# Optimization experiments

Hardware: AMD Instinct MI355X
Metric: run time of the kernel (lower is better)

The kernel has to match this reference:

```python
import jax, jax.numpy as jnp
import numpy as np


def setup_inputs() -> dict:
    key = jax.random.key(0)
    k1, k2 = jax.random.split(key)
    B, C, D = 16384, 4096, 1024
    feat = jax.random.normal(k1, (B, D), dtype=jnp.float32)
    centers = jax.random.normal(k2, (C, D), dtype=jnp.float32)
    return {"feat": feat, "centers": centers}


def reference(feat, centers):
    # Pairwise squared Euclidean distance: dist[b, c] = sum_d (feat[b,d] - centers[c,d])^2
    # materializing the O(B*C*D) broadcast difference (same math as the torch module).
    x2 = jnp.sum(feat * feat, axis=-1, keepdims=True)          # [B, 1]
    c2 = jnp.sum(centers * centers, axis=-1)[None, :]          # [1, C]
    xc = jnp.einsum("bd,cd->bc", feat, centers)                # [B, C] GEMM
    dist = x2 + c2 - 2.0 * xc
    return dist
```

## Files before the change

kernel.cpp:

```cpp
#include <hip/hip_runtime.h>
#include <hip/hip_bf16.h>

typedef __bf16 bf16x8 __attribute__((ext_vector_type(8)));
typedef float floatx4 __attribute__((ext_vector_type(4)));

__device__ __forceinline__ unsigned short f2bf(float f) {
    unsigned u = __float_as_uint(f);
    u += 0x7FFFu + ((u >> 16) & 1u);
    return (unsigned short)(u >> 16);
}

__device__ __forceinline__ void gl2lds(const void* g, void* l) {
    void* gnc = const_cast<void*>(g);
    __builtin_amdgcn_global_load_lds(
        (__attribute__((address_space(1))) void*)gnc,
        (__attribute__((address_space(3))) void*)l,
        16, 0, 0);
}

__global__ __launch_bounds__(256) void cast_norm_kernel(
    const float* __restrict__ in, unsigned short* __restrict__ outb,
    float* __restrict__ norm)
{
    const int row = blockIdx.x;
    const int tid = threadIdx.x;
    const float4 v = ((const float4*)(in + (size_t)row * 1024))[tid];
    float s = v.x * v.x + v.y * v.y + v.z * v.z + v.w * v.w;
    ushort4 o;
    o.x = f2bf(v.x); o.y = f2bf(v.y); o.z = f2bf(v.z); o.w = f2bf(v.w);
    ((ushort4*)(outb + (size_t)row * 1024))[tid] = o;
#pragma unroll
    for (int off = 32; off > 0; off >>= 1) s += __shfl_down(s, off);
    __shared__ float ws[4];
    if ((tid & 63) == 0) ws[tid >> 6] = s;
    __syncthreads();
    if (tid == 0) norm[row] = ws[0] + ws[1] + ws[2] + ws[3];
}

__global__ __launch_bounds__(256) void dist_gemm(
    const unsigned short* __restrict__ A,
    const unsigned short* __restrict__ B,
    const float* __restrict__ x2,
    const float* __restrict__ c2,
    float* __restrict__ out,
    int M, int N)
{
    constexpr int K = 1024;
    __shared__ unsigned short sA[128 * 32];
    __shared__ unsigned short sB[128 * 32];

    const int tid  = threadIdx.x;
    const int wave = tid >> 6;
    const int lane = tid & 63;
    const int quad = lane >> 4;
    const int l16  = lane & 15;
    const int wm   = wave & 1;
    const int wn   = wave >> 1;

    const int blockRow = blockIdx.y * 128;
    const int blockCol = blockIdx.x * 128;

    const int srow = lane >> 2;
    const int scol = (lane & 3) * 8;

    unsigned short* ldsA0 = sA + wave * 512;
    unsigned short* ldsA1 = sA + (wave + 4) * 512;
    unsigned short* ldsB0 = sB + wave * 512;
    unsigned short* ldsB1 = sB + (wave + 4) * 512;

    const unsigned short* gA0 = A + (size_t)(blockRow + wave * 16 + srow) * K + scol;
    const unsigned short* gA1 = A + (size_t)(blockRow + (wave + 4) * 16 + srow) * K + scol;
    const unsigned short* gB0 = B + (size_t)(blockCol + wave * 16 + srow) * K + scol;
    const unsigned short* gB1 = B + (size_t)(blockCol + (wave + 4) * 16 + srow) * K + scol;

    floatx4 acc[4][4];
#pragma unroll
    for (int i = 0; i < 4; i++)
#pragma unroll
        for (int j = 0; j < 4; j++) acc[i][j] = (floatx4){0.f, 0.f, 0.f, 0.f};

    const bf16x8* fragA[4];
    const bf16x8* fragB[4];
#pragma unroll
    for (int i = 0; i < 4; i++) {
        fragA[i] = (const bf16x8*)(sA + ((wm * 64 + i * 16 + l16) * 32 + quad * 8));
        fragB[i] = (const bf16x8*)(sB + ((wn * 64 + i * 16 + l16) * 32 + quad * 8));
    }

    for (int k0 = 0; k0 < K; k0 += 32) {
        __syncthreads();
        gl2lds(gA0 + k0, ldsA0);
        gl2lds(gA1 + k0, ldsA1);
        gl2lds(gB0 + k0, ldsB0);
        gl2lds(gB1 + k0, ldsB1);
        __syncthreads();

        bf16x8 a[4], b[4];
#pragma unroll
        for (int i = 0; i < 4; i++) a[i] = *fragA[i];
#pragma unroll
        for (int j = 0; j < 4; j++) b[j] = *fragB[j];
#pragma unroll
        for (int i = 0; i < 4; i++)
#pragma unroll
            for (int j = 0; j < 4; j++)
                acc[i][j] = __builtin_amdgcn_mfma_f32_16x16x32_bf16(a[i], b[j], acc[i][j], 0, 0, 0);
    }

    float c2v[4];
#pragma unroll
    for (int j = 0; j < 4; j++) c2v[j] = c2[blockCol + wn * 64 + j * 16 + l16];

#pragma unroll
    for (int i = 0; i < 4; i++) {
        const int rowb = blockRow + wm * 64 + i * 16 + quad * 4;
        float x2v[4];
#pragma unroll
        for (int r = 0; r < 4; r++) x2v[r] = x2[rowb + r];
#pragma unroll
        for (int j = 0; j < 4; j++) {
            const int col = blockCol + wn * 64 + j * 16 + l16;
            float* o = out + (size_t)rowb * N + col;
#pragma unroll
            for (int r = 0; r < 4; r++)
                o[(size_t)r * N] = fmaf(-2.0f, acc[i][j][r], x2v[r] + c2v[j]);
        }
    }
}

__global__ __launch_bounds__(256) void dist_fallback(
    const float* __restrict__ A, const float* __restrict__ B,
    float* __restrict__ out, int M, int N, int K)
{
    __shared__ float sA[64][17];
    __shared__ float sB[64][17];
    const int tid = threadIdx.x;
    const int tx = tid & 15;
    const int ty = tid >> 4;
    const int rowBase = blockIdx.y * 64;
    const int colBase = blockIdx.x * 64;
    float acc[4][4] = {};
    for (int k0 = 0; k0 < K; k0 += 16) {
        __syncthreads();
        {
            const int r = tid >> 2, c = (tid & 3) * 4;
            float4 va = *(const float4*)(A + (size_t)(rowBase + r) * K + k0 + c);
            sA[r][c] = va.x; sA[r][c + 1] = va.y; sA[r][c + 2] = va.z; sA[r][c + 3] = va.w;
            float4 vb = *(const float4*)(B + (size_t)(colBase + r) * K + k0 + c);
            sB[r][c] = vb.x; sB[r][c + 1] = vb.y; sB[r][c + 2] = vb.z; sB[r][c + 3] = vb.w;
        }
        __syncthreads();
#pragma unroll
        for (int kk = 0; kk < 16; kk++) {
            float ra[4], rb[4];
#pragma unroll
            for (int i = 0; i < 4; i++) ra[i] = sA[ty * 4 + i][kk];
#pragma unroll
            for (int j = 0; j < 4; j++) rb[j] = sB[tx * 4 + j][kk];
#pragma unroll
            for (int i = 0; i < 4; i++)
#pragma unroll
                for (int j = 0; j < 4; j++) {
                    float d = ra[i] - rb[j];
                    acc[i][j] = fmaf(d, d, acc[i][j]);
                }
        }
    }
#pragma unroll
    for (int i = 0; i < 4; i++)
#pragma unroll
        for (int j = 0; j < 4; j++)
            out[(size_t)(rowBase + ty * 4 + i) * N + (colBase + tx * 4 + j)] = acc[i][j];
}

extern "C" void kernel_launch(void* const* d_in, const int* in_sizes, int n_in,
                              void* d_out, int out_size, void* d_ws, size_t ws_size,
                              hipStream_t stream) {
    const float* feat = (const float*)d_in[0];
    const float* cent = (const float*)d_in[1];
    float* out = (float*)d_out;

    const int D = 1024;
    const int M = in_sizes[0] / D;
    const int N = in_sizes[1] / D;

    const size_t offA  = 0;
    const size_t offB  = offA + (size_t)M * D * sizeof(unsigned short);
    const size_t offX2 = offB + (size_t)N * D * sizeof(unsigned short);
    const size_t offC2 = offX2 + (size_t)M * sizeof(float);
    const size_t need  = offC2 + (size_t)N * sizeof(float);

    if (ws_size >= need && (M % 128) == 0 && (N % 128) == 0) {
        unsigned short* Ab = (unsigned short*)((char*)d_ws + offA);
        unsigned short* Bb = (unsigned short*)((char*)d_ws + offB);
        float* x2 = (float*)((char*)d_ws + offX2);
        float* c2 = (float*)((char*)d_ws + offC2);

        cast_norm_kernel<<<M, 256, 0, stream>>>(feat, Ab, x2);
        cast_norm_kernel<<<N, 256, 0, stream>>>(cent, Bb, c2);
        dist_gemm<<<dim3(N / 128, M / 128), 256, 0, stream>>>(Ab, Bb, x2, c2, out, M, N);
    } else {
        dist_fallback<<<dim3(N / 64, M / 64), 256, 0, stream>>>(feat, cent, out, M, N, D);
    }
}
```

Before: 472.5 us.

## Fuse cast-norm launches, swizzle GEMM tiles, use nontemporal output stores

Replaces the two per-matrix cast/norm launches with a single kernel that handles two rows per block and writes packed 16-byte bf16 stores. Remaps GEMM block indices into 8x8 supertiles so neighbouring blocks share A and B tiles in L2. Writes the large fp32 output with nontemporal stores so it does not pollute the cache. The fast path now requires M and N to be multiples of 1024, which sends more shapes to the slow fallback.

Result: slower. 483.3 us (+2.3%).

```diff
diff --git a/kernel.cpp b/kernel.cpp
--- a/kernel.cpp
+++ b/kernel.cpp
@@ -4,10 +4,10 @@
 typedef __bf16 bf16x8 __attribute__((ext_vector_type(8)));
 typedef float floatx4 __attribute__((ext_vector_type(4)));
 
-__device__ __forceinline__ unsigned short f2bf(float f) {
+__device__ __forceinline__ unsigned f2bf(float f) {
     unsigned u = __float_as_uint(f);
     u += 0x7FFFu + ((u >> 16) & 1u);
-    return (unsigned short)(u >> 16);
+    return u >> 16;
 }
 
 __device__ __forceinline__ void gl2lds(const void* g, void* l) {
@@ -18,23 +18,48 @@
         16, 0, 0);
 }
 
-__global__ __launch_bounds__(256) void cast_norm_kernel(
-    const float* __restrict__ in, unsigned short* __restrict__ outb,
-    float* __restrict__ norm)
+__global__ __launch_bounds__(256) void cast_norm2(
+    const float* __restrict__ feat, const float* __restrict__ cent,
+    unsigned short* __restrict__ Ab, unsigned short* __restrict__ Bb,
+    float* __restrict__ x2, float* __restrict__ c2, int M)
 {
-    const int row = blockIdx.x;
-    const int tid = threadIdx.x;
-    const float4 v = ((const float4*)(in + (size_t)row * 1024))[tid];
-    float s = v.x * v.x + v.y * v.y + v.z * v.z + v.w * v.w;
-    ushort4 o;
-    o.x = f2bf(v.x); o.y = f2bf(v.y); o.z = f2bf(v.z); o.w = f2bf(v.w);
-    ((ushort4*)(outb + (size_t)row * 1024))[tid] = o;
+    const int tid  = threadIdx.x;
+    const int half = tid >> 7;
+    const int t    = tid & 127;
+    const int row  = blockIdx.x * 2 + half;
+
+    const float* src;
+    unsigned short* dst;
+    float* nrm;
+    if (row < M) {
+        src = feat + (size_t)row * 1024;
+        dst = Ab   + (size_t)row * 1024;
+        nrm = x2 + row;
+    } else {
+        const int r = row - M;
+        src = cent + (size_t)r * 1024;
+        dst = Bb   + (size_t)r * 1024;
+        nrm = c2 + r;
+    }
+
+    const float4 v0 = ((const float4*)src)[t * 2];
+    const float4 v1 = ((const float4*)src)[t * 2 + 1];
+    float s = v0.x * v0.x + v0.y * v0.y + v0.z * v0.z + v0.w * v0.w
+            + v1.x * v1.x + v1.y * v1.y + v1.z * v1.z + v1.w * v1.w;
+
+    uint4 o;
+    o.x = f2bf(v0.x) | (f2bf(v0.y) << 16);
+    o.y = f2bf(v0.z) | (f2bf(v0.w) << 16);
+    o.z = f2bf(v1.x) | (f2bf(v1.y) << 16);
+    o.w = f2bf(v1.z) | (f2bf(v1.w) << 16);
+    ((uint4*)dst)[t] = o;
+
 #pragma unroll
     for (int off = 32; off > 0; off >>= 1) s += __shfl_down(s, off);
     __shared__ float ws[4];
     if ((tid & 63) == 0) ws[tid >> 6] = s;
     __syncthreads();
-    if (tid == 0) norm[row] = ws[0] + ws[1] + ws[2] + ws[3];
+    if (t == 0) *nrm = ws[half * 2] + ws[half * 2 + 1];
 }
 
 __global__ __launch_bounds__(256) void dist_gemm(
@@ -57,8 +82,16 @@
     const int wm   = wave & 1;
     const int wn   = wave >> 1;
 
-    const int blockRow = blockIdx.y * 128;
-    const int blockCol = blockIdx.x * 128;
+    const int gx = gridDim.x;
+    const int lin = blockIdx.y * gx + blockIdx.x;
+    const int tilesPerRow = gx >> 3;
+    const int super  = lin >> 6;
+    const int within = lin & 63;
+    const int bx = (super % tilesPerRow) * 8 + (within & 7);
+    const int by = (super / tilesPerRow) * 8 + (within >> 3);
+
+    const int blockRow = by * 128;
+    const int blockCol = bx * 128;
 
     const int srow = lane >> 2;
     const int scol = (lane & 3) * 8;
@@ -123,7 +156,8 @@
             float* o = out + (size_t)rowb * N + col;
 #pragma unroll
             for (int r = 0; r < 4; r++)
-                o[(size_t)r * N] = fmaf(-2.0f, acc[i][j][r], x2v[r] + c2v[j]);
+                __builtin_nontemporal_store(
+                    fmaf(-2.0f, acc[i][j][r], x2v[r] + c2v[j]), o + (size_t)r * N);
         }
     }
 }
@@ -190,14 +224,13 @@
     const size_t offC2 = offX2 + (size_t)M * sizeof(float);
     const size_t need  = offC2 + (size_t)N * sizeof(float);
 
-    if (ws_size >= need && (M % 128) == 0 && (N % 128) == 0) {
+    if (ws_size >= need && (M % 1024) == 0 && (N % 1024) == 0) {
         unsigned short* Ab = (unsigned short*)((char*)d_ws + offA);
         unsigned short* Bb = (unsigned short*)((char*)d_ws + offB);
         float* x2 = (float*)((char*)d_ws + offX2);
         float* c2 = (float*)((char*)d_ws + offC2);
 
-        cast_norm_kernel<<<M, 256, 0, stream>>>(feat, Ab, x2);
-        cast_norm_kernel<<<N, 256, 0, stream>>>(cent, Bb, c2);
+        cast_norm2<<<(M + N) / 2, 256, 0, stream>>>(feat, cent, Ab, Bb, x2, c2, M);
         dist_gemm<<<dim3(N / 128, M / 128), 256, 0, stream>>>(Ab, Bb, x2, c2, out, M, N);
     } else {
         dist_fallback<<<dim3(N / 64, M / 64), 256, 0, stream>>>(feat, cent, out, M, N, D);
```
